# Kernel tuning notes

Measured on AMD Instinct MI355X. Metric: run time of the kernel, lower is better.

Reference implementation:

```python
import jax, jax.numpy as jnp
import numpy as np

NUM_HEADS = 16
HEAD_DIM = 64  # v_emb_out // num_heads


def setup_inputs() -> dict:
    key = jax.random.key(0)
    ks = jax.random.split(key, 12)
    B, QL, KL = 2, 2048, 2048
    D = 1024  # q_emb_in = k_emb_in = v_emb_in = v_emb_out
    s = 0.02
    return {
        "q": jax.random.normal(ks[0], (B, QL, D), jnp.float32),
        "k": jax.random.normal(ks[1], (B, KL, D), jnp.float32),
        "v": jax.random.normal(ks[2], (B, KL, D), jnp.float32),
        "mask": jnp.zeros((B, 1, 1, KL), jnp.int32),
        "Wq": jax.random.normal(ks[3], (D, D), jnp.float32) * s,
        "bq": jnp.zeros((D,), jnp.float32),
        "Wk": jax.random.normal(ks[4], (D, D), jnp.float32) * s,
        "bk": jnp.zeros((D,), jnp.float32),
        "Wv": jax.random.normal(ks[5], (D, D), jnp.float32) * s,
        "bv": jnp.zeros((D,), jnp.float32),
        "Wo": jax.random.normal(ks[6], (D, D), jnp.float32) * s,
        "bo": jnp.zeros((D,), jnp.float32),
    }


def _split_heads(x):
    # (B, S, D) -> (B, H, S, Hd)
    B, S, D = x.shape
    return x.reshape(B, S, NUM_HEADS, HEAD_DIM).transpose(0, 2, 1, 3)


def reference(q, k, v, mask, Wq, bq, Wk, bk, Wv, bv, Wo, bo):
    Q = _split_heads(q @ Wq.T + bq)
    K = _split_heads(k @ Wk.T + bk)
    V = _split_heads(v @ Wv.T + bv)
    scores = jnp.einsum("bhqd,bhkd->bhqk", Q, K) / jnp.sqrt(
        jnp.asarray(HEAD_DIM, Q.dtype)
    )
    scores = jnp.where(mask.astype(bool), jnp.asarray(-jnp.inf, scores.dtype), scores)
    attn = jax.nn.softmax(scores, axis=-1)
    out = jnp.einsum("bhqk,bhkd->bhqd", attn, V)  # (B,H,Q,Hd)
    B, H, QL, Hd = out.shape
    out = out.transpose(0, 2, 1, 3).reshape(B, QL, H * Hd)
    return out @ Wo.T + bo
```

## Files before the change

### kernel.cpp

```cpp
#include <hip/hip_runtime.h>
#include <hip/hip_bf16.h>
#include <math.h>
#include <stdint.h>


typedef __bf16 bf16x8 __attribute__((ext_vector_type(8)));
typedef float  f32x4  __attribute__((ext_vector_type(4)));
typedef float  f32x8  __attribute__((ext_vector_type(8)));
typedef unsigned short u16x8 __attribute__((ext_vector_type(8)));
typedef unsigned short u16x4 __attribute__((ext_vector_type(4)));
typedef u16x8 u16x8a __attribute__((may_alias));
typedef u16x4 u16x4a __attribute__((may_alias));
typedef f32x8 f32x8a __attribute__((may_alias));
typedef unsigned short u16a __attribute__((may_alias));
typedef float f32a __attribute__((may_alias));

#define BATCH 2
#define SQL   2048
#define DM    1024
#define NH    16
#define HD    64

__device__ __forceinline__ unsigned short f2bf(float f) {
    union { __hip_bfloat16 h; unsigned short u; } cv;
    cv.h = __float2bfloat16(f);
    return cv.u;
}
__device__ __forceinline__ float bf2f(unsigned short u) {
    union { unsigned int i; float f; } cv;
    cv.i = ((unsigned int)u) << 16;
    return cv.f;
}
__device__ __forceinline__ bf16x8 ldfrag(const unsigned short* p) {
    return __builtin_bit_cast(bf16x8, *(const u16x8a*)p);
}
__device__ __forceinline__ void stage8(const void* __restrict__ src, size_t off,
                                       int f32f, unsigned short* dst) {
    if (f32f) {
        f32x8 v = *(const f32x8a*)((const float*)src + off);
        u16x8 o;
#pragma unroll
        for (int i = 0; i < 8; i++) o[i] = f2bf(v[i]);
        *(u16x8a*)dst = o;
    } else {
        *(u16x8a*)dst = *(const u16x8a*)((const unsigned short*)src + off);
    }
}
__device__ __forceinline__ float rdel(const void* p, size_t i, int f) {
    return f ? ((const f32a*)p)[i] : bf2f(((const u16a*)p)[i]);
}
__device__ __forceinline__ void gload16(const void* g, void* l) {
    __builtin_amdgcn_global_load_lds(
        (const __attribute__((address_space(1))) unsigned int*)g,
        (__attribute__((address_space(3))) unsigned int*)l,
        16, 0, 0);
}

__global__ void sniff(const void* __restrict__ q, int* __restrict__ flag) {
    __shared__ int cnt;
    if (threadIdx.x == 0) cnt = 0;
    __syncthreads();
    const u16a* p = (const u16a*)q;
    int c = 0;
#pragma unroll
    for (int i = 0; i < 8; i++) {
        unsigned short u = p[threadIdx.x * 8 + i];
        int e = (u >> 7) & 0xFF;
        if (e >= 96 && e <= 159) c++;
    }
    atomicAdd(&cnt, c);
    __syncthreads();
    if (threadIdx.x == 0) *flag = (cnt < 1741) ? 1 : 0;
}

__global__ __launch_bounds__(256)
void convert(const void* s0, const void* s1, const void* s2, const void* s3,
             const void* s4, const void* s5, const void* s6,
             unsigned short* d0, unsigned short* d1, unsigned short* d2,
             unsigned short* d3, unsigned short* d4, unsigned short* d5,
             unsigned short* d6, const int* __restrict__ flag)
{
    if (*flag == 0) return;
    const int z = blockIdx.z;
    const float* s; unsigned short* d; size_t n;
    switch (z) {
        case 0: s = (const float*)s0; d = d0; n = (size_t)BATCH * SQL * DM; break;
        case 1: s = (const float*)s1; d = d1; n = (size_t)BATCH * SQL * DM; break;
        case 2: s = (const float*)s2; d = d2; n = (size_t)BATCH * SQL * DM; break;
        case 3: s = (const float*)s3; d = d3; n = (size_t)DM * DM; break;
        case 4: s = (const float*)s4; d = d4; n = (size_t)DM * DM; break;
        case 5: s = (const float*)s5; d = d5; n = (size_t)DM * DM; break;
        default: s = (const float*)s6; d = d6; n = (size_t)DM * DM; break;
    }
    const size_t stride = (size_t)gridDim.x * blockDim.x * 8;
    for (size_t i = ((size_t)blockIdx.x * blockDim.x + threadIdx.x) * 8; i < n;
         i += stride) {
        f32x8 v = *(const f32x8a*)(s + i);
        u16x8 o;
#pragma unroll
        for (int j = 0; j < 8; j++) o[j] = f2bf(v[j]);
        *(u16x8a*)(d + i) = o;
    }
}

template<int BLDS, int BN>
__device__ __forceinline__ void gemm_core(
    const unsigned short* __restrict__ Abf,
    const unsigned short* __restrict__ Bbf,
    const void* __restrict__ Braw,
    const void* __restrict__ bias, void* __restrict__ Cv,
    float scale, int wF32, int oMode, int bF32)
{
    constexpr int K = 1024, N = 1024, BK = 32;
    constexpr int NJ = BN / 32;
    constexpr int CALLS = BN / 64;
    __shared__ unsigned short Alds[128 * BK];
    __shared__ unsigned short Blds[BN * BK];

    const int t = threadIdx.x;
    const int lane = t & 63, wave = t >> 6;
    const int quad = lane >> 4, r15 = lane & 15;
    const int wm = (wave >> 1) * 64, wn = (wave & 1) * (BN / 2);
    const int m0 = blockIdx.x * 128, n0 = blockIdx.y * BN;

    f32x4 acc[4][NJ];
#pragma unroll
    for (int i = 0; i < 4; i++)
#pragma unroll
        for (int j = 0; j < NJ; j++) acc[i][j] = (f32x4){0.f, 0.f, 0.f, 0.f};

    const int gr = lane >> 2, gc = lane & 3;
    const unsigned short* gA = Abf + (size_t)(m0 + wave * 32 + gr) * K + gc * 8;
    const unsigned short* gB = Bbf + (size_t)(n0 + wave * 16 * CALLS + gr) * K + gc * 8;
    unsigned short* lA = &Alds[wave * 1024];
    unsigned short* lB = &Blds[wave * 512 * CALLS];
    const int srow = t >> 2, sch = t & 3;
    const size_t offB0 = (size_t)(n0 + srow) * K + sch * 8;
    const size_t offB1 = (size_t)(n0 + 64 + srow) * K + sch * 8;

    for (int k0 = 0; k0 < K; k0 += BK) {
        gload16(gA + k0, lA);
        gload16(gA + k0 + 16 * K, lA + 512);
        if constexpr (BLDS) {
#pragma unroll
            for (int c = 0; c < CALLS; c++)
                gload16(gB + k0 + c * 16 * K, lB + c * 512);
        } else {
            stage8(Braw, offB0 + k0, wF32, &Blds[srow * BK + sch * 8]);
            if constexpr (BN == 128)
                stage8(Braw, offB1 + k0, wF32, &Blds[(64 + srow) * BK + sch * 8]);
        }
        __syncthreads();

        bf16x8 af[4], bfr[NJ];
#pragma unroll
        for (int i = 0; i < 4; i++)
            af[i] = ldfrag(&Alds[(wm + i * 16 + r15) * BK + quad * 8]);
#pragma unroll
        for (int j = 0; j < NJ; j++)
            bfr[j] = ldfrag(&Blds[(wn + j * 16 + r15) * BK + quad * 8]);
#pragma unroll
        for (int i = 0; i < 4; i++)
#pragma unroll
            for (int j = 0; j < NJ; j++)
                acc[i][j] = __builtin_amdgcn_mfma_f32_16x16x32_bf16(af[i], bfr[j], acc[i][j], 0, 0, 0);
        __syncthreads();
    }

    float bvv[NJ];
#pragma unroll
    for (int j = 0; j < NJ; j++)
        bvv[j] = rdel(bias, n0 + wn + j * 16 + r15, bF32);

    if (oMode == 2) {
#pragma unroll
        for (int i = 0; i < 4; i++)
#pragma unroll
            for (int j = 0; j < NJ; j++) {
                int rr = m0 + wm + i * 16 + quad * 4;
                int cc = n0 + wn + j * 16 + r15;
                int bb = rr >> 11, tok = rr & (SQL - 1);
                int hh = cc >> 6,  dd  = cc & (HD - 1);
                u16x4 pk;
#pragma unroll
                for (int r = 0; r < 4; r++) pk[r] = f2bf(acc[i][j][r] + bvv[j]);
                *(u16x4a*)&((u16a*)Cv)[((((size_t)bb * NH + hh) * HD + dd) << 11) + tok] = pk;
            }
    } else {
#pragma unroll
        for (int i = 0; i < 4; i++)
#pragma unroll
            for (int j = 0; j < NJ; j++)
#pragma unroll
                for (int r = 0; r < 4; r++) {
                    int rr = m0 + wm + i * 16 + quad * 4 + r;
                    int cc = n0 + wn + j * 16 + r15;
                    float vv = (acc[i][j][r] + bvv[j]) * scale;
                    if (oMode) ((f32a*)Cv)[(size_t)rr * N + cc] = vv;
                    else       ((u16a*)Cv)[(size_t)rr * N + cc] = f2bf(vv);
                }
    }
}

template<int BLDS>
__global__ __launch_bounds__(256)
void gemm_qkv_k(const void* __restrict__ xq, const void* __restrict__ xk,
                const void* __restrict__ xv,
                const unsigned short* __restrict__ qc,
                const unsigned short* __restrict__ kc,
                const unsigned short* __restrict__ vc,
                const void* __restrict__ Wq, const void* __restrict__ Wk,
                const void* __restrict__ Wv,
                const unsigned short* __restrict__ Wqc,
                const unsigned short* __restrict__ Wkc,
                const unsigned short* __restrict__ Wvc,
                const void* __restrict__ bq, const void* __restrict__ bk,
                const void* __restrict__ bv,
                unsigned short* __restrict__ Qp, unsigned short* __restrict__ Kp,
                unsigned short* __restrict__ Vp,
                float qscale, const int* __restrict__ flag)
{
    const int f = *flag;
    const int z = blockIdx.z;
    const void* xo = (z == 0) ? xq : (z == 1) ? xk : xv;
    const unsigned short* xc = (z == 0) ? qc : (z == 1) ? kc : vc;
    const unsigned short* A = f ? xc : (const unsigned short*)xo;
    const void* Wraw = (z == 0) ? Wq : (z == 1) ? Wk : Wv;
    const unsigned short* Wc = (z == 0) ? Wqc : (z == 1) ? Wkc : Wvc;
    const unsigned short* Bc = (BLDS && f) ? Wc : (const unsigned short*)Wraw;
    const void* bi = (z == 0) ? bq : (z == 1) ? bk : bv;
    unsigned short* C = (z == 0) ? Qp : (z == 1) ? Kp : Vp;
    gemm_core<BLDS, 128>(A, Bc, Wraw, bi, C, (z == 0) ? qscale : 1.0f, f,
                         (z == 2) ? 2 : 0, f);
}

template<int BLDS>
__global__ __launch_bounds__(256)
void gemm_o_k(const unsigned short* __restrict__ A, const void* __restrict__ Wo,
              const unsigned short* __restrict__ Woc, const void* __restrict__ bo,
              void* __restrict__ out, const int* __restrict__ flag)
{
    const int f = *flag;
    const unsigned short* Bc = (BLDS && f) ? Woc : (const unsigned short*)Wo;
    gemm_core<BLDS, 64>(A, Bc, Wo, bo, out, 1.0f, f, f, f);
}

__global__ __launch_bounds__(256)
void flash(const unsigned short* __restrict__ Qp,
           const unsigned short* __restrict__ Kp,
           const unsigned short* __restrict__ VT,
           const int* __restrict__ mask,
           unsigned short* __restrict__ AO)
{
    __shared__ unsigned short Klds[2][64 * 64];
    __shared__ unsigned short Vlds[2][64 * 64];
    __shared__ unsigned short Plds[4][32 * 72];

    const int t = threadIdx.x, wave = t >> 6, lane = t & 63;
    const int quad = lane >> 4, r15 = lane & 15;
    const int x7 = r15 & 7;
    const int qt = blockIdx.x, bh = blockIdx.y, b = bh >> 4, h = bh & 15;
    const size_t base = (size_t)b * SQL * DM + (size_t)h * HD;

    const int srow8 = lane >> 3, sc8 = lane & 7;
    const unsigned short* gK[2];
    const unsigned short* gV[2];
    int ldof[2];
#pragma unroll
    for (int i = 0; i < 2; i++) {
        const int row = wave * 16 + i * 8 + srow8;
        const int slot = sc8 ^ (row & 7);
        gK[i] = Kp + base + (size_t)row * DM + slot * 8;
        gV[i] = VT + (((size_t)(b * NH + h) * HD + row) << 11) + slot * 8;
        ldof[i] = (wave * 16 + i * 8) * 64;
    }

    bf16x8 qf[2][2];
#pragma unroll
    for (int g = 0; g < 2; g++) {
        const int qrow = qt * 128 + wave * 32 + g * 16 + r15;
        qf[g][0] = ldfrag(&Qp[base + (size_t)qrow * DM + quad * 8]);
        qf[g][1] = ldfrag(&Qp[base + (size_t)qrow * DM + 32 + quad * 8]);
    }

    f32x4 o[2][4];
#pragma unroll
    for (int g = 0; g < 2; g++)
#pragma unroll
        for (int jd = 0; jd < 4; jd++) o[g][jd] = (f32x4){0.f, 0.f, 0.f, 0.f};
    float l_i[2][4] = {{0.f, 0.f, 0.f, 0.f}, {0.f, 0.f, 0.f, 0.f}};

#pragma unroll
    for (int i = 0; i < 2; i++) {
        gload16(gK[i], &Klds[0][ldof[i]]);
        gload16(gV[i], &Vlds[0][ldof[i]]);
    }
    __syncthreads();

    constexpr int NT = SQL / 64;
    for (int it = 0; it < NT; ++it) {
        const int bs = it & 1;
        const int n0 = it * 64;

        int mraw[4];
#pragma unroll
        for (int j = 0; j < 4; j++)
            mraw[j] = mask[b * SQL + n0 + j * 16 + r15];

        if (it + 1 < NT) {
#pragma unroll
            for (int i = 0; i < 2; i++) {
                gload16(gK[i] + (size_t)(n0 + 64) * DM, &Klds[bs ^ 1][ldof[i]]);
                gload16(gV[i] + (n0 + 64),              &Vlds[bs ^ 1][ldof[i]]);
            }
        }

        f32x4 s4[2][4];
#pragma unroll
        for (int g = 0; g < 2; g++)
#pragma unroll
            for (int j = 0; j < 4; j++) s4[g][j] = (f32x4){0.f, 0.f, 0.f, 0.f};
#pragma unroll
        for (int j = 0; j < 4; j++) {
            const int row = j * 16 + r15;
            bf16x8 kf0 = ldfrag(&Klds[bs][row * 64 + ((quad ^ x7) << 3)]);
            bf16x8 kf1 = ldfrag(&Klds[bs][row * 64 + (((4 + quad) ^ x7) << 3)]);
#pragma unroll
            for (int g = 0; g < 2; g++) {
                s4[g][j] = __builtin_amdgcn_mfma_f32_16x16x32_bf16(qf[g][0], kf0, s4[g][j], 0, 0, 0);
                s4[g][j] = __builtin_amdgcn_mfma_f32_16x16x32_bf16(qf[g][1], kf1, s4[g][j], 0, 0, 0);
            }
        }

#pragma unroll
        for (int j = 0; j < 4; j++) {
            const float mval = (mraw[j] != 0) ? -INFINITY : 0.f;
#pragma unroll
            for (int g = 0; g < 2; g++)
#pragma unroll
                for (int r = 0; r < 4; r++) {
                    float p = exp2f(s4[g][j][r] + mval);
                    l_i[g][r] += p;
                    Plds[wave][(g * 16 + quad * 4 + r) * 72 + j * 16 + r15] = f2bf(p);
                }
        }
        asm volatile("" ::: "memory");

#pragma unroll
        for (int kf = 0; kf < 2; kf++) {
            bf16x8 pa0 = ldfrag(&Plds[wave][(r15) * 72 + kf * 32 + quad * 8]);
            bf16x8 pa1 = ldfrag(&Plds[wave][(16 + r15) * 72 + kf * 32 + quad * 8]);
#pragma unroll
            for (int jd = 0; jd < 4; jd++) {
                const int row = jd * 16 + r15;
                bf16x8 vb8 = ldfrag(
                    &Vlds[bs][row * 64 + (((kf * 4 + quad) ^ x7) << 3)]);
                o[0][jd] = __builtin_amdgcn_mfma_f32_16x16x32_bf16(pa0, vb8, o[0][jd], 0, 0, 0);
                o[1][jd] = __builtin_amdgcn_mfma_f32_16x16x32_bf16(pa1, vb8, o[1][jd], 0, 0, 0);
            }
        }
        __syncthreads();
    }

#pragma unroll
    for (int off = 1; off < 16; off <<= 1)
#pragma unroll
        for (int g = 0; g < 2; g++)
#pragma unroll
            for (int r = 0; r < 4; r++)
                l_i[g][r] += __shfl_xor(l_i[g][r], off, 64);
#pragma unroll
    for (int g = 0; g < 2; g++)
#pragma unroll
        for (int r = 0; r < 4; r++)
            l_i[g][r] = (l_i[g][r] > 0.f) ? 1.0f / l_i[g][r] : 0.f;

#pragma unroll
    for (int g = 0; g < 2; g++)
#pragma unroll
        for (int jd = 0; jd < 4; jd++)
#pragma unroll
            for (int r = 0; r < 4; r++) {
                int row = qt * 128 + wave * 32 + g * 16 + quad * 4 + r;
                AO[base + (size_t)row * DM + jd * 16 + r15] =
                    f2bf(o[g][jd][r] * l_i[g][r]);
            }
}

extern "C" void kernel_launch(void* const* d_in, const int* in_sizes, int n_in,
                              void* d_out, int out_size, void* d_ws, size_t ws_size,
                              hipStream_t stream)
{
    (void)in_sizes; (void)n_in; (void)out_size;

    const void* q    = d_in[0];
    const void* k    = d_in[1];
    const void* v    = d_in[2];
    const int*  mask = (const int*)d_in[3];
    const void* Wq   = d_in[4];
    const void* bq   = d_in[5];
    const void* Wk   = d_in[6];
    const void* bk   = d_in[7];
    const void* Wv   = d_in[8];
    const void* bv   = d_in[9];
    const void* Wo   = d_in[10];
    const void* bo   = d_in[11];

    const size_t ACT = (size_t)BATCH * SQL * DM;
    const size_t WE  = (size_t)DM * DM;
    int* flag = (int*)d_ws;
    unsigned short* Qp = (unsigned short*)((char*)d_ws + 512);
    unsigned short* Kp = Qp + ACT;
    unsigned short* Vp = Kp + ACT;
    unsigned short* AO = Vp + ACT;

    const size_t needFull = 512 + (4 * ACT + 3 * ACT + 4 * WE) * 2;
    const size_t needMid  = 512 + (4 * ACT + 4 * WE) * 2;
    const int tier = (ws_size >= needFull) ? 2 : (ws_size >= needMid) ? 1 : 0;

    unsigned short* qc;
    unsigned short* kc;
    unsigned short* vc;
    unsigned short* Wqc = AO + ACT;
    unsigned short* Wkc = Wqc + WE;
    unsigned short* Wvc = Wkc + WE;
    unsigned short* Woc = Wvc + WE;
    if (tier == 2) {
        qc = Woc + WE;
        kc = qc + ACT;
        vc = kc + ACT;
    } else {
        qc = AO;
        kc = (unsigned short*)d_out;
        vc = kc + ACT;
    }

    const float QSCALE = 0.125f * 1.44269504088896340736f;

    sniff<<<1, 256, 0, stream>>>(q, flag);
    if (tier >= 1) {
        convert<<<dim3(256, 1, 7), 256, 0, stream>>>(
            q, k, v, Wq, Wk, Wv, Wo, qc, kc, vc, Wqc, Wkc, Wvc, Woc, flag);
        gemm_qkv_k<1><<<dim3(32, 8, 3), 256, 0, stream>>>(
            q, k, v, qc, kc, vc, Wq, Wk, Wv, Wqc, Wkc, Wvc,
            bq, bk, bv, Qp, Kp, Vp, QSCALE, flag);
    } else {
        convert<<<dim3(256, 1, 3), 256, 0, stream>>>(
            q, k, v, nullptr, nullptr, nullptr, nullptr,
            qc, kc, vc, nullptr, nullptr, nullptr, nullptr, flag);
        gemm_qkv_k<0><<<dim3(32, 8, 3), 256, 0, stream>>>(
            q, k, v, qc, kc, vc, Wq, Wk, Wv, nullptr, nullptr, nullptr,
            bq, bk, bv, Qp, Kp, Vp, QSCALE, flag);
    }
    flash<<<dim3(SQL / 128, BATCH * NH), 256, 0, stream>>>(Qp, Kp, Vp, mask, AO);
    if (tier >= 1)
        gemm_o_k<1><<<dim3(32, 16), 256, 0, stream>>>(AO, Wo, Woc, bo, d_out, flag);
    else
        gemm_o_k<0><<<dim3(32, 16), 256, 0, stream>>>(AO, Wo, nullptr, bo, d_out, flag);
}
```

Measured before the change: 255.0 us.

## Alias bf16 conversion buffers into workspace regions and always use LDS B-loads

Removes the workspace-size tiers and the register-staged B path, reusing dead regions of Qp/Vp/AO/output as scratch for the converted weights and activations so the direct-to-LDS B load path always runs. To make the aliasing safe, the QKV GEMM is split into a Q/K launch and a separate V launch with its own weight conversion, and Wo is converted after flash attention. This adds extra kernel launches and a smaller tile for the V projection in exchange for avoiding the slow fallback when the workspace is small.

```diff
diff --git a/kernel.cpp b/kernel.cpp
--- a/kernel.cpp
+++ b/kernel.cpp
@@ -20,6 +20,8 @@
 #define DM    1024
 #define NH    16
 #define HD    64
+#define ACTN  ((size_t)BATCH * SQL * DM)
+#define WEN   ((size_t)DM * DM)
 
 __device__ __forceinline__ unsigned short f2bf(float f) {
     union { __hip_bfloat16 h; unsigned short u; } cv;
@@ -33,18 +35,6 @@
 }
 __device__ __forceinline__ bf16x8 ldfrag(const unsigned short* p) {
     return __builtin_bit_cast(bf16x8, *(const u16x8a*)p);
-}
-__device__ __forceinline__ void stage8(const void* __restrict__ src, size_t off,
-                                       int f32f, unsigned short* dst) {
-    if (f32f) {
-        f32x8 v = *(const f32x8a*)((const float*)src + off);
-        u16x8 o;
-#pragma unroll
-        for (int i = 0; i < 8; i++) o[i] = f2bf(v[i]);
-        *(u16x8a*)dst = o;
-    } else {
-        *(u16x8a*)dst = *(const u16x8a*)((const unsigned short*)src + off);
-    }
 }
 __device__ __forceinline__ float rdel(const void* p, size_t i, int f) {
     return f ? ((const f32a*)p)[i] : bf2f(((const u16a*)p)[i]);
@@ -74,42 +64,55 @@
 }
 
 __global__ __launch_bounds__(256)
-void convert(const void* s0, const void* s1, const void* s2, const void* s3,
-             const void* s4, const void* s5, const void* s6,
-             unsigned short* d0, unsigned short* d1, unsigned short* d2,
-             unsigned short* d3, unsigned short* d4, unsigned short* d5,
-             unsigned short* d6, const int* __restrict__ flag)
+void convertA(const void* q, const void* k, const void* v,
+              const void* Wq, const void* Wk,
+              unsigned short* qc, unsigned short* kc, unsigned short* vc,
+              unsigned short* Wqc, unsigned short* Wkc,
+              const int* __restrict__ flag)
 {
     if (*flag == 0) return;
     const int z = blockIdx.z;
     const float* s; unsigned short* d; size_t n;
     switch (z) {
-        case 0: s = (const float*)s0; d = d0; n = (size_t)BATCH * SQL * DM; break;
-        case 1: s = (const float*)s1; d = d1; n = (size_t)BATCH * SQL * DM; break;
-        case 2: s = (const float*)s2; d = d2; n = (size_t)BATCH * SQL * DM; break;
-        case 3: s = (const float*)s3; d = d3; n = (size_t)DM * DM; break;
-        case 4: s = (const float*)s4; d = d4; n = (size_t)DM * DM; break;
-        case 5: s = (const float*)s5; d = d5; n = (size_t)DM * DM; break;
-        default: s = (const float*)s6; d = d6; n = (size_t)DM * DM; break;
+        case 0: s = (const float*)q;  d = qc;  n = ACTN; break;
+        case 1: s = (const float*)k;  d = kc;  n = ACTN; break;
+        case 2: s = (const float*)v;  d = vc;  n = ACTN; break;
+        case 3: s = (const float*)Wq; d = Wqc; n = WEN;  break;
+        default: s = (const float*)Wk; d = Wkc; n = WEN; break;
     }
     const size_t stride = (size_t)gridDim.x * blockDim.x * 8;
     for (size_t i = ((size_t)blockIdx.x * blockDim.x + threadIdx.x) * 8; i < n;
          i += stride) {
-        f32x8 v = *(const f32x8a*)(s + i);
+        f32x8 vv = *(const f32x8a*)(s + i);
         u16x8 o;
 #pragma unroll
-        for (int j = 0; j < 8; j++) o[j] = f2bf(v[j]);
+        for (int j = 0; j < 8; j++) o[j] = f2bf(vv[j]);
         *(u16x8a*)(d + i) = o;
     }
 }
 
-template<int BLDS, int BN>
+__global__ __launch_bounds__(256)
+void convertW(const void* s_, unsigned short* d, const int* __restrict__ flag)
+{
+    if (*flag == 0) return;
+    const float* s = (const float*)s_;
+    const size_t stride = (size_t)gridDim.x * blockDim.x * 8;
+    for (size_t i = ((size_t)blockIdx.x * blockDim.x + threadIdx.x) * 8;
+         i < WEN; i += stride) {
+        f32x8 vv = *(const f32x8a*)(s + i);
+        u16x8 o;
+#pragma unroll
+        for (int j = 0; j < 8; j++) o[j] = f2bf(vv[j]);
+        *(u16x8a*)(d + i) = o;
+    }
+}
+
+template<int BN>
 __device__ __forceinline__ void gemm_core(
     const unsigned short* __restrict__ Abf,
     const unsigned short* __restrict__ Bbf,
-    const void* __restrict__ Braw,
     const void* __restrict__ bias, void* __restrict__ Cv,
-    float scale, int wF32, int oMode, int bF32)
+    float scale, int oMode, int bF32)
 {
     constexpr int K = 1024, N = 1024, BK = 32;
     constexpr int NJ = BN / 32;
@@ -134,22 +137,13 @@
     const unsigned short* gB = Bbf + (size_t)(n0 + wave * 16 * CALLS + gr) * K + gc * 8;
     unsigned short* lA = &Alds[wave * 1024];
     unsigned short* lB = &Blds[wave * 512 * CALLS];
-    const int srow = t >> 2, sch = t & 3;
-    const size_t offB0 = (size_t)(n0 + srow) * K + sch * 8;
-    const size_t offB1 = (size_t)(n0 + 64 + srow) * K + sch * 8;
 
     for (int k0 = 0; k0 < K; k0 += BK) {
         gload16(gA + k0, lA);
         gload16(gA + k0 + 16 * K, lA + 512);
-        if constexpr (BLDS) {
-#pragma unroll
-            for (int c = 0; c < CALLS; c++)
-                gload16(gB + k0 + c * 16 * K, lB + c * 512);
-        } else {
-            stage8(Braw, offB0 + k0, wF32, &Blds[srow * BK + sch * 8]);
-            if constexpr (BN == 128)
-                stage8(Braw, offB1 + k0, wF32, &Blds[(64 + srow) * BK + sch * 8]);
-        }
+#pragma unroll
+        for (int c = 0; c < CALLS; c++)
+            gload16(gB + k0 + c * 16 * K, lB + c * 512);
         __syncthreads();
 
         bf16x8 af[4], bfr[NJ];
@@ -202,47 +196,46 @@
     }
 }
 
-template<int BLDS>
-__global__ __launch_bounds__(256)
-void gemm_qkv_k(const void* __restrict__ xq, const void* __restrict__ xk,
-                const void* __restrict__ xv,
-                const unsigned short* __restrict__ qc,
-                const unsigned short* __restrict__ kc,
-                const unsigned short* __restrict__ vc,
-                const void* __restrict__ Wq, const void* __restrict__ Wk,
-                const void* __restrict__ Wv,
-                const unsigned short* __restrict__ Wqc,
-                const unsigned short* __restrict__ Wkc,
-                const unsigned short* __restrict__ Wvc,
-                const void* __restrict__ bq, const void* __restrict__ bk,
-                const void* __restrict__ bv,
-                unsigned short* __restrict__ Qp, unsigned short* __restrict__ Kp,
-                unsigned short* __restrict__ Vp,
-                float qscale, const int* __restrict__ flag)
+__global__ __launch_bounds__(256)
+void gemm_qk(const void* __restrict__ xq, const void* __restrict__ xk,
+             const unsigned short* __restrict__ qc,
+             const unsigned short* __restrict__ kc,
+             const void* __restrict__ Wq, const void* __restrict__ Wk,
+             const unsigned short* __restrict__ Wqc,
+             const unsigned short* __restrict__ Wkc,
+             const void* __restrict__ bq, const void* __restrict__ bk,
+             unsigned short* __restrict__ Qp, unsigned short* __restrict__ Kp,
+             float qscale, const int* __restrict__ flag)
 {
     const int f = *flag;
     const int z = blockIdx.z;
-    const void* xo = (z == 0) ? xq : (z == 1) ? xk : xv;
-    const unsigned short* xc = (z == 0) ? qc : (z == 1) ? kc : vc;
-    const unsigned short* A = f ? xc : (const unsigned short*)xo;
-    const void* Wraw = (z == 0) ? Wq : (z == 1) ? Wk : Wv;
-    const unsigned short* Wc = (z == 0) ? Wqc : (z == 1) ? Wkc : Wvc;
-    const unsigned short* Bc = (BLDS && f) ? Wc : (const unsigned short*)Wraw;
-    const void* bi = (z == 0) ? bq : (z == 1) ? bk : bv;
-    unsigned short* C = (z == 0) ? Qp : (z == 1) ? Kp : Vp;
-    gemm_core<BLDS, 128>(A, Bc, Wraw, bi, C, (z == 0) ? qscale : 1.0f, f,
-                         (z == 2) ? 2 : 0, f);
-}
-
-template<int BLDS>
-__global__ __launch_bounds__(256)
-void gemm_o_k(const unsigned short* __restrict__ A, const void* __restrict__ Wo,
-              const unsigned short* __restrict__ Woc, const void* __restrict__ bo,
-              void* __restrict__ out, const int* __restrict__ flag)
+    const unsigned short* A =
+        f ? (z ? kc : qc) : (const unsigned short*)(z ? xk : xq);
+    const unsigned short* B =
+        f ? (z ? Wkc : Wqc) : (const unsigned short*)(z ? Wk : Wq);
+    gemm_core<128>(A, B, z ? bk : bq, z ? Kp : Qp, z ? 1.0f : qscale, 0, f);
+}
+
+__global__ __launch_bounds__(256)
+void gemm_v(const void* __restrict__ xv, const unsigned short* __restrict__ vc,
+            const void* __restrict__ Wv, const unsigned short* __restrict__ Wvc,
+            const void* __restrict__ bv, unsigned short* __restrict__ VT,
+            const int* __restrict__ flag)
 {
     const int f = *flag;
-    const unsigned short* Bc = (BLDS && f) ? Woc : (const unsigned short*)Wo;
-    gemm_core<BLDS, 64>(A, Bc, Wo, bo, out, 1.0f, f, f, f);
+    const unsigned short* A = f ? vc : (const unsigned short*)xv;
+    const unsigned short* B = f ? Wvc : (const unsigned short*)Wv;
+    gemm_core<64>(A, B, bv, VT, 1.0f, 2, f);
+}
+
+__global__ __launch_bounds__(256)
+void gemm_o(const unsigned short* __restrict__ AO, const void* __restrict__ Wo,
+            const unsigned short* __restrict__ Woc, const void* __restrict__ bo,
+            void* __restrict__ out, const int* __restrict__ flag)
+{
+    const int f = *flag;
+    const unsigned short* B = f ? Woc : (const unsigned short*)Wo;
+    gemm_core<64>(AO, B, bo, out, 1.0f, f, f);
 }
 
 __global__ __launch_bounds__(256)
@@ -391,7 +384,7 @@
                               void* d_out, int out_size, void* d_ws, size_t ws_size,
                               hipStream_t stream)
 {
-    (void)in_sizes; (void)n_in; (void)out_size;
+    (void)in_sizes; (void)n_in; (void)out_size; (void)ws_size;
 
     const void* q    = d_in[0];
     const void* k    = d_in[1];
@@ -406,55 +399,30 @@
     const void* Wo   = d_in[10];
     const void* bo   = d_in[11];
 
-    const size_t ACT = (size_t)BATCH * SQL * DM;
-    const size_t WE  = (size_t)DM * DM;
     int* flag = (int*)d_ws;
     unsigned short* Qp = (unsigned short*)((char*)d_ws + 512);
-    unsigned short* Kp = Qp + ACT;
-    unsigned short* Vp = Kp + ACT;
-    unsigned short* AO = Vp + ACT;
-
-    const size_t needFull = 512 + (4 * ACT + 3 * ACT + 4 * WE) * 2;
-    const size_t needMid  = 512 + (4 * ACT + 4 * WE) * 2;
-    const int tier = (ws_size >= needFull) ? 2 : (ws_size >= needMid) ? 1 : 0;
-
-    unsigned short* qc;
-    unsigned short* kc;
-    unsigned short* vc;
-    unsigned short* Wqc = AO + ACT;
-    unsigned short* Wkc = Wqc + WE;
-    unsigned short* Wvc = Wkc + WE;
-    unsigned short* Woc = Wvc + WE;
-    if (tier == 2) {
-        qc = Woc + WE;
-        kc = qc + ACT;
-        vc = kc + ACT;
-    } else {
-        qc = AO;
-        kc = (unsigned short*)d_out;
-        vc = kc + ACT;
-    }
+    unsigned short* Kp = Qp + ACTN;
+    unsigned short* Vp = Kp + ACTN;
+    unsigned short* AO = Vp + ACTN;
+
+    unsigned short* qc  = AO;
+    unsigned short* kc  = (unsigned short*)d_out;
+    unsigned short* vc  = kc + ACTN;
+    unsigned short* Wqc = Vp;
+    unsigned short* Wkc = Vp + WEN;
+    unsigned short* Wvc = AO;
+    unsigned short* Woc = Qp;
 
     const float QSCALE = 0.125f * 1.44269504088896340736f;
 
     sniff<<<1, 256, 0, stream>>>(q, flag);
-    if (tier >= 1) {
-        convert<<<dim3(256, 1, 7), 256, 0, stream>>>(
-            q, k, v, Wq, Wk, Wv, Wo, qc, kc, vc, Wqc, Wkc, Wvc, Woc, flag);
-        gemm_qkv_k<1><<<dim3(32, 8, 3), 256, 0, stream>>>(
-            q, k, v, qc, kc, vc, Wq, Wk, Wv, Wqc, Wkc, Wvc,
-            bq, bk, bv, Qp, Kp, Vp, QSCALE, flag);
-    } else {
-        convert<<<dim3(256, 1, 3), 256, 0, stream>>>(
-            q, k, v, nullptr, nullptr, nullptr, nullptr,
-            qc, kc, vc, nullptr, nullptr, nullptr, nullptr, flag);
-        gemm_qkv_k<0><<<dim3(32, 8, 3), 256, 0, stream>>>(
-            q, k, v, qc, kc, vc, Wq, Wk, Wv, nullptr, nullptr, nullptr,
-            bq, bk, bv, Qp, Kp, Vp, QSCALE, flag);
-    }
+    convertA<<<dim3(256, 1, 5), 256, 0, stream>>>(
+        q, k, v, Wq, Wk, qc, kc, vc, Wqc, Wkc, flag);
+    gemm_qk<<<dim3(32, 8, 2), 256, 0, stream>>>(
+        q, k, qc, kc, Wq, Wk, Wqc, Wkc, bq, bk, Qp, Kp, QSCALE, flag);
+    convertW<<<dim3(256), 256, 0, stream>>>(Wv, Wvc, flag);
+    gemm_v<<<dim3(32, 16), 256, 0, stream>>>(v, vc, Wv, Wvc, bv, Vp, flag);
     flash<<<dim3(SQL / 128, BATCH * NH), 256, 0, stream>>>(Qp, Kp, Vp, mask, AO);
-    if (tier >= 1)
-        gemm_o_k<1><<<dim3(32, 16), 256, 0, stream>>>(AO, Wo, Woc, bo, d_out, flag);
-    else
-        gemm_o_k<0><<<dim3(32, 16), 256, 0, stream>>>(AO, Wo, nullptr, bo, d_out, flag);
-}
+    convertW<<<dim3(256), 256, 0, stream>>>(Wo, Woc, flag);
+    gemm_o<<<dim3(32, 16), 256, 0, stream>>>(AO, Wo, Woc, bo, d_out, flag);
+}
```

Measured after the change: 277.7 us. +8.9%, slower.

## Double-buffer GEMM LDS tiles to overlap global loads with MFMA

Applied to the files above, without the earlier changes.

Splits the A and B shared-memory tiles into two buffers and prefetches the next K-slice into the alternate buffer while MFMAs run on the current one. This drops one barrier per iteration and aims to hide global-to-LDS load latency behind compute. It doubles LDS use per block, which may lower occupancy. The synchronous stage8 path still blocks on its loads before writing to LDS, so overlap there is limited.

```diff
diff --git a/kernel.cpp b/kernel.cpp
--- a/kernel.cpp
+++ b/kernel.cpp
@@ -114,8 +114,8 @@
     constexpr int K = 1024, N = 1024, BK = 32;
     constexpr int NJ = BN / 32;
     constexpr int CALLS = BN / 64;
-    __shared__ unsigned short Alds[128 * BK];
-    __shared__ unsigned short Blds[BN * BK];
+    __shared__ unsigned short Alds[2][128 * BK];
+    __shared__ unsigned short Blds[2][BN * BK];
 
     const int t = threadIdx.x;
     const int lane = t & 63, wave = t >> 6;
@@ -132,33 +132,52 @@
     const int gr = lane >> 2, gc = lane & 3;
     const unsigned short* gA = Abf + (size_t)(m0 + wave * 32 + gr) * K + gc * 8;
     const unsigned short* gB = Bbf + (size_t)(n0 + wave * 16 * CALLS + gr) * K + gc * 8;
-    unsigned short* lA = &Alds[wave * 1024];
-    unsigned short* lB = &Blds[wave * 512 * CALLS];
+    const int lAo = wave * 1024;
+    const int lBo = wave * 512 * CALLS;
     const int srow = t >> 2, sch = t & 3;
     const size_t offB0 = (size_t)(n0 + srow) * K + sch * 8;
     const size_t offB1 = (size_t)(n0 + 64 + srow) * K + sch * 8;
 
-    for (int k0 = 0; k0 < K; k0 += BK) {
-        gload16(gA + k0, lA);
-        gload16(gA + k0 + 16 * K, lA + 512);
-        if constexpr (BLDS) {
-#pragma unroll
-            for (int c = 0; c < CALLS; c++)
-                gload16(gB + k0 + c * 16 * K, lB + c * 512);
-        } else {
-            stage8(Braw, offB0 + k0, wF32, &Blds[srow * BK + sch * 8]);
-            if constexpr (BN == 128)
-                stage8(Braw, offB1 + k0, wF32, &Blds[(64 + srow) * BK + sch * 8]);
+    gload16(gA, &Alds[0][lAo]);
+    gload16(gA + 16 * K, &Alds[0][lAo + 512]);
+    if constexpr (BLDS) {
+#pragma unroll
+        for (int c = 0; c < CALLS; c++)
+            gload16(gB + c * 16 * K, &Blds[0][lBo + c * 512]);
+    } else {
+        stage8(Braw, offB0, wF32, &Blds[0][srow * BK + sch * 8]);
+        if constexpr (BN == 128)
+            stage8(Braw, offB1, wF32, &Blds[0][(64 + srow) * BK + sch * 8]);
+    }
+    __syncthreads();
+
+    constexpr int NSTEP = K / BK;
+    for (int s = 0; s < NSTEP; ++s) {
+        const int cur = s & 1;
+        if (s + 1 < NSTEP) {
+            const int k0n = (s + 1) * BK;
+            gload16(gA + k0n, &Alds[cur ^ 1][lAo]);
+            gload16(gA + k0n + 16 * K, &Alds[cur ^ 1][lAo + 512]);
+            if constexpr (BLDS) {
+#pragma unroll
+                for (int c = 0; c < CALLS; c++)
+                    gload16(gB + k0n + c * 16 * K, &Blds[cur ^ 1][lBo + c * 512]);
+            } else {
+                stage8(Braw, offB0 + k0n, wF32,
+                       &Blds[cur ^ 1][srow * BK + sch * 8]);
+                if constexpr (BN == 128)
+                    stage8(Braw, offB1 + k0n, wF32,
+                           &Blds[cur ^ 1][(64 + srow) * BK + sch * 8]);
+            }
         }
-        __syncthreads();
 
         bf16x8 af[4], bfr[NJ];
 #pragma unroll
         for (int i = 0; i < 4; i++)
-            af[i] = ldfrag(&Alds[(wm + i * 16 + r15) * BK + quad * 8]);
+            af[i] = ldfrag(&Alds[cur][(wm + i * 16 + r15) * BK + quad * 8]);
 #pragma unroll
         for (int j = 0; j < NJ; j++)
-            bfr[j] = ldfrag(&Blds[(wn + j * 16 + r15) * BK + quad * 8]);
+            bfr[j] = ldfrag(&Blds[cur][(wn + j * 16 + r15) * BK + quad * 8]);
 #pragma unroll
         for (int i = 0; i < 4; i++)
 #pragma unroll
```

Result: slower. 262.6 us (+3.0%).

## Software-pipeline projection GEMM K-loop with multi-buffered LDS and register-staged B

Applied to the files above, without the earlier changes.

Replaces the single-buffered GEMM main loop with a software pipeline. A tiles use a triple-buffered LDS ring filled by direct global-to-LDS loads two steps ahead. B tiles are prefetched into registers and written into a double-buffered LDS slot one step ahead. Explicit vmcnt waits and barriers let global loads overlap the MFMA work instead of stalling on two syncthreads per step. The cost is more LDS per block, more registers for the staged B data, and hand-placed waitcnt counts that must exactly match the number of outstanding loads.

```diff
diff --git a/kernel.cpp b/kernel.cpp
--- a/kernel.cpp
+++ b/kernel.cpp
@@ -33,18 +33,6 @@
 }
 __device__ __forceinline__ bf16x8 ldfrag(const unsigned short* p) {
     return __builtin_bit_cast(bf16x8, *(const u16x8a*)p);
-}
-__device__ __forceinline__ void stage8(const void* __restrict__ src, size_t off,
-                                       int f32f, unsigned short* dst) {
-    if (f32f) {
-        f32x8 v = *(const f32x8a*)((const float*)src + off);
-        u16x8 o;
-#pragma unroll
-        for (int i = 0; i < 8; i++) o[i] = f2bf(v[i]);
-        *(u16x8a*)dst = o;
-    } else {
-        *(u16x8a*)dst = *(const u16x8a*)((const unsigned short*)src + off);
-    }
 }
 __device__ __forceinline__ float rdel(const void* p, size_t i, int f) {
     return f ? ((const f32a*)p)[i] : bf2f(((const u16a*)p)[i]);
@@ -103,69 +91,139 @@
     }
 }
 
-template<int BLDS, int BN>
-__device__ __forceinline__ void gemm_core(
+template<int WF32> struct BRegSel { using T = f32x8; };
+template<> struct BRegSel<0> { using T = u16x8; };
+
+template<int BN, int WF32>
+__device__ __forceinline__ void kloop(
+    unsigned short* __restrict__ Al,
+    unsigned short* __restrict__ Bl,
     const unsigned short* __restrict__ Abf,
-    const unsigned short* __restrict__ Bbf,
-    const void* __restrict__ Braw,
-    const void* __restrict__ bias, void* __restrict__ Cv,
-    float scale, int wF32, int oMode, int bF32)
-{
-    constexpr int K = 1024, N = 1024, BK = 32;
-    constexpr int NJ = BN / 32;
-    constexpr int CALLS = BN / 64;
-    __shared__ unsigned short Alds[128 * BK];
-    __shared__ unsigned short Blds[BN * BK];
-
-    const int t = threadIdx.x;
-    const int lane = t & 63, wave = t >> 6;
+    const void* __restrict__ Bv,
+    f32x4 (&acc)[4][BN / 32], int m0, int n0)
+{
+    constexpr int K = 1024, BK = 32, NJ = BN / 32, NSTEP = K / BK;
+    constexpr int ABUF = 128 * BK, BBUF = BN * BK;
+    constexpr int SV = (BN == 128) ? (WF32 ? 6 : 4) : (WF32 ? 4 : 3);
+    using BR = typename BRegSel<WF32>::T;
+
+    const int tid = threadIdx.x;
+    const int lane = tid & 63, wave = tid >> 6;
     const int quad = lane >> 4, r15 = lane & 15;
     const int wm = (wave >> 1) * 64, wn = (wave & 1) * (BN / 2);
-    const int m0 = blockIdx.x * 128, n0 = blockIdx.y * BN;
-
-    f32x4 acc[4][NJ];
-#pragma unroll
-    for (int i = 0; i < 4; i++)
-#pragma unroll
-        for (int j = 0; j < NJ; j++) acc[i][j] = (f32x4){0.f, 0.f, 0.f, 0.f};
-
     const int gr = lane >> 2, gc = lane & 3;
     const unsigned short* gA = Abf + (size_t)(m0 + wave * 32 + gr) * K + gc * 8;
-    const unsigned short* gB = Bbf + (size_t)(n0 + wave * 16 * CALLS + gr) * K + gc * 8;
-    unsigned short* lA = &Alds[wave * 1024];
-    unsigned short* lB = &Blds[wave * 512 * CALLS];
-    const int srow = t >> 2, sch = t & 3;
+    const int lAo = wave * 1024;
+    const int srow = tid >> 2, sch = tid & 3;
     const size_t offB0 = (size_t)(n0 + srow) * K + sch * 8;
     const size_t offB1 = (size_t)(n0 + 64 + srow) * K + sch * 8;
 
-    for (int k0 = 0; k0 < K; k0 += BK) {
-        gload16(gA + k0, lA);
-        gload16(gA + k0 + 16 * K, lA + 512);
-        if constexpr (BLDS) {
-#pragma unroll
-            for (int c = 0; c < CALLS; c++)
-                gload16(gB + k0 + c * 16 * K, lB + c * 512);
+    auto bload = [&](BR& r0, BR& r1, int kk) {
+        if constexpr (WF32) {
+            r0 = *(const f32x8a*)((const float*)Bv + offB0 + kk);
+            if constexpr (BN == 128)
+                r1 = *(const f32x8a*)((const float*)Bv + offB1 + kk);
         } else {
-            stage8(Braw, offB0 + k0, wF32, &Blds[srow * BK + sch * 8]);
+            r0 = *(const u16x8a*)((const unsigned short*)Bv + offB0 + kk);
             if constexpr (BN == 128)
-                stage8(Braw, offB1 + k0, wF32, &Blds[(64 + srow) * BK + sch * 8]);
+                r1 = *(const u16x8a*)((const unsigned short*)Bv + offB1 + kk);
         }
-        __syncthreads();
-
-        bf16x8 af[4], bfr[NJ];
-#pragma unroll
-        for (int i = 0; i < 4; i++)
-            af[i] = ldfrag(&Alds[(wm + i * 16 + r15) * BK + quad * 8]);
-#pragma unroll
-        for (int j = 0; j < NJ; j++)
-            bfr[j] = ldfrag(&Blds[(wn + j * 16 + r15) * BK + quad * 8]);
-#pragma unroll
-        for (int i = 0; i < 4; i++)
-#pragma unroll
-            for (int j = 0; j < NJ; j++)
-                acc[i][j] = __builtin_amdgcn_mfma_f32_16x16x32_bf16(af[i], bfr[j], acc[i][j], 0, 0, 0);
-        __syncthreads();
-    }
+        (void)r1;
+    };
+    auto bwrite = [&](const BR& r0, const BR& r1, unsigned short* dst) {
+        if constexpr (WF32) {
+            u16x8 o0;
+#pragma unroll
+            for (int i = 0; i < 8; i++) o0[i] = f2bf(r0[i]);
+            *(u16x8a*)&dst[srow * BK + sch * 8] = o0;
+            if constexpr (BN == 128) {
+                u16x8 o1;
+#pragma unroll
+                for (int i = 0; i < 8; i++) o1[i] = f2bf(r1[i]);
+                *(u16x8a*)&dst[(64 + srow) * BK + sch * 8] = o1;
+            }
+        } else {
+            *(u16x8a*)&dst[srow * BK + sch * 8] = __builtin_bit_cast(u16x8, r0);
+            if constexpr (BN == 128)
+                *(u16x8a*)&dst[(64 + srow) * BK + sch * 8] =
+                    __builtin_bit_cast(u16x8, r1);
+        }
+        (void)r1;
+    };
+    auto vmsteady = []() {
+        if constexpr (SV == 6)      asm volatile("s_waitcnt vmcnt(6)" ::: "memory");
+        else if constexpr (SV == 4) asm volatile("s_waitcnt vmcnt(4)" ::: "memory");
+        else                        asm volatile("s_waitcnt vmcnt(3)" ::: "memory");
+    };
+
+    BR rA0{}, rA1{}, rB0{}, rB1{};
+
+    gload16(gA, Al + lAo);
+    gload16(gA + 16 * K, Al + lAo + 512);
+    bload(rA0, rA1, 0);
+    gload16(gA + BK, Al + ABUF + lAo);
+    gload16(gA + BK + 16 * K, Al + ABUF + lAo + 512);
+    bload(rB0, rB1, BK);
+    __builtin_amdgcn_sched_barrier(0);
+    vmsteady();
+    __builtin_amdgcn_sched_barrier(0);
+    bwrite(rA0, rA1, Bl);
+
+#define GSTEP(T_, L0_, L1_, W0_, W1_)                                         \
+    {                                                                         \
+        asm volatile("s_waitcnt lgkmcnt(0)" ::: "memory");                    \
+        __builtin_amdgcn_s_barrier();                                         \
+        __builtin_amdgcn_sched_barrier(0);                                    \
+        const unsigned short* Ab_ = Al + ((T_) % 3) * ABUF;                   \
+        const unsigned short* Bb_ = Bl + ((T_) & 1) * BBUF;                   \
+        bf16x8 af_[4], bf_[NJ];                                               \
+        _Pragma("unroll")                                                     \
+        for (int i = 0; i < 4; i++)                                           \
+            af_[i] = ldfrag(&Ab_[(wm + i * 16 + r15) * BK + quad * 8]);       \
+        _Pragma("unroll")                                                     \
+        for (int j = 0; j < NJ; j++)                                          \
+            bf_[j] = ldfrag(&Bb_[(wn + j * 16 + r15) * BK + quad * 8]);       \
+        _Pragma("unroll")                                                     \
+        for (int i = 0; i < 4; i++)                                           \
+            _Pragma("unroll")                                                 \
+            for (int j = 0; j < NJ; j++)                                      \
+                acc[i][j] = __builtin_amdgcn_mfma_f32_16x16x32_bf16(          \
+                    af_[i], bf_[j], acc[i][j], 0, 0, 0);                      \
+        __builtin_amdgcn_s_barrier();                                         \
+        __builtin_amdgcn_sched_barrier(0);                                    \
+        if ((T_) + 2 < NSTEP) {                                               \
+            const int k2_ = ((T_) + 2) * BK;                                  \
+            unsigned short* Ad_ = Al + (((T_) + 2) % 3) * ABUF;               \
+            gload16(gA + k2_, Ad_ + lAo);                                     \
+            gload16(gA + k2_ + 16 * K, Ad_ + lAo + 512);                      \
+            bload(L0_, L1_, k2_);                                             \
+            __builtin_amdgcn_sched_barrier(0);                                \
+            vmsteady();                                                       \
+            __builtin_amdgcn_sched_barrier(0);                                \
+        } else if ((T_) + 1 < NSTEP) {                                        \
+            asm volatile("s_waitcnt vmcnt(0)" ::: "memory");                  \
+        }                                                                     \
+        if ((T_) + 1 < NSTEP)                                                 \
+            bwrite(W0_, W1_, Bl + (((T_) + 1) & 1) * BBUF);                   \
+    }
+
+    for (int t = 0; t < NSTEP; t += 2) {
+        GSTEP(t,     rA0, rA1, rB0, rB1);
+        GSTEP(t + 1, rB0, rB1, rA0, rA1);
+    }
+#undef GSTEP
+}
+
+template<int BN>
+__device__ __forceinline__ void epilog(
+    f32x4 (&acc)[4][BN / 32], const void* __restrict__ bias,
+    void* __restrict__ Cv, float scale, int oMode, int bF32, int m0, int n0)
+{
+    constexpr int N = 1024, NJ = BN / 32;
+    const int tid = threadIdx.x;
+    const int lane = tid & 63, wave = tid >> 6;
+    const int quad = lane >> 4, r15 = lane & 15;
+    const int wm = (wave >> 1) * 64, wn = (wave & 1) * (BN / 2);
 
     float bvv[NJ];
 #pragma unroll
@@ -202,24 +260,26 @@
     }
 }
 
-template<int BLDS>
 __global__ __launch_bounds__(256)
-void gemm_qkv_k(const void* __restrict__ xq, const void* __restrict__ xk,
-                const void* __restrict__ xv,
-                const unsigned short* __restrict__ qc,
-                const unsigned short* __restrict__ kc,
-                const unsigned short* __restrict__ vc,
-                const void* __restrict__ Wq, const void* __restrict__ Wk,
-                const void* __restrict__ Wv,
-                const unsigned short* __restrict__ Wqc,
-                const unsigned short* __restrict__ Wkc,
-                const unsigned short* __restrict__ Wvc,
-                const void* __restrict__ bq, const void* __restrict__ bk,
-                const void* __restrict__ bv,
-                unsigned short* __restrict__ Qp, unsigned short* __restrict__ Kp,
-                unsigned short* __restrict__ Vp,
-                float qscale, const int* __restrict__ flag)
-{
+void gemm_qkv(const void* __restrict__ xq, const void* __restrict__ xk,
+              const void* __restrict__ xv,
+              const unsigned short* __restrict__ qc,
+              const unsigned short* __restrict__ kc,
+              const unsigned short* __restrict__ vc,
+              const void* __restrict__ Wq, const void* __restrict__ Wk,
+              const void* __restrict__ Wv,
+              const unsigned short* __restrict__ Wqc,
+              const unsigned short* __restrict__ Wkc,
+              const unsigned short* __restrict__ Wvc,
+              const void* __restrict__ bq, const void* __restrict__ bk,
+              const void* __restrict__ bv,
+              unsigned short* __restrict__ Qp, unsigned short* __restrict__ Kp,
+              unsigned short* __restrict__ Vp,
+              float qscale, const int* __restrict__ flag, int useWc)
+{
+    __shared__ unsigned short Al[3 * 128 * 32];
+    __shared__ unsigned short Bl[2 * 128 * 32];
+
     const int f = *flag;
     const int z = blockIdx.z;
     const void* xo = (z == 0) ? xq : (z == 1) ? xk : xv;
@@ -227,22 +287,45 @@
     const unsigned short* A = f ? xc : (const unsigned short*)xo;
     const void* Wraw = (z == 0) ? Wq : (z == 1) ? Wk : Wv;
     const unsigned short* Wc = (z == 0) ? Wqc : (z == 1) ? Wkc : Wvc;
-    const unsigned short* Bc = (BLDS && f) ? Wc : (const unsigned short*)Wraw;
     const void* bi = (z == 0) ? bq : (z == 1) ? bk : bv;
     unsigned short* C = (z == 0) ? Qp : (z == 1) ? Kp : Vp;
-    gemm_core<BLDS, 128>(A, Bc, Wraw, bi, C, (z == 0) ? qscale : 1.0f, f,
-                         (z == 2) ? 2 : 0, f);
-}
-
-template<int BLDS>
+    const float scale = (z == 0) ? qscale : 1.0f;
+    const int oMode = (z == 2) ? 2 : 0;
+    const int m0 = blockIdx.x * 128, n0 = blockIdx.y * 128;
+
+    f32x4 acc[4][4];
+#pragma unroll
+    for (int i = 0; i < 4; i++)
+#pragma unroll
+        for (int j = 0; j < 4; j++) acc[i][j] = (f32x4){0.f, 0.f, 0.f, 0.f};
+
+    if (f && !useWc)      kloop<128, 1>(Al, Bl, A, Wraw, acc, m0, n0);
+    else if (f)           kloop<128, 0>(Al, Bl, A, Wc,   acc, m0, n0);
+    else                  kloop<128, 0>(Al, Bl, A, Wraw, acc, m0, n0);
+    epilog<128>(acc, bi, C, scale, oMode, f, m0, n0);
+}
+
 __global__ __launch_bounds__(256)
-void gemm_o_k(const unsigned short* __restrict__ A, const void* __restrict__ Wo,
-              const unsigned short* __restrict__ Woc, const void* __restrict__ bo,
-              void* __restrict__ out, const int* __restrict__ flag)
-{
+void gemm_o(const unsigned short* __restrict__ A, const void* __restrict__ Wo,
+            const unsigned short* __restrict__ Woc, const void* __restrict__ bo,
+            void* __restrict__ out, const int* __restrict__ flag, int useWc)
+{
+    __shared__ unsigned short Al[3 * 128 * 32];
+    __shared__ unsigned short Bl[2 * 64 * 32];
+
     const int f = *flag;
-    const unsigned short* Bc = (BLDS && f) ? Woc : (const unsigned short*)Wo;
-    gemm_core<BLDS, 64>(A, Bc, Wo, bo, out, 1.0f, f, f, f);
+    const int m0 = blockIdx.x * 128, n0 = blockIdx.y * 64;
+
+    f32x4 acc[4][2];
+#pragma unroll
+    for (int i = 0; i < 4; i++)
+#pragma unroll
+        for (int j = 0; j < 2; j++) acc[i][j] = (f32x4){0.f, 0.f, 0.f, 0.f};
+
+    if (f && !useWc)      kloop<64, 1>(Al, Bl, A, Wo,  acc, m0, n0);
+    else if (f)           kloop<64, 0>(Al, Bl, A, Woc, acc, m0, n0);
+    else                  kloop<64, 0>(Al, Bl, A, Wo,  acc, m0, n0);
+    epilog<64>(acc, bo, out, 1.0f, f, f, m0, n0);
 }
 
 __global__ __launch_bounds__(256)
@@ -434,27 +517,22 @@
         kc = (unsigned short*)d_out;
         vc = kc + ACT;
     }
+    const int useWc = (tier >= 1) ? 1 : 0;
 
     const float QSCALE = 0.125f * 1.44269504088896340736f;
 
     sniff<<<1, 256, 0, stream>>>(q, flag);
-    if (tier >= 1) {
+    if (useWc) {
         convert<<<dim3(256, 1, 7), 256, 0, stream>>>(
             q, k, v, Wq, Wk, Wv, Wo, qc, kc, vc, Wqc, Wkc, Wvc, Woc, flag);
-        gemm_qkv_k<1><<<dim3(32, 8, 3), 256, 0, stream>>>(
-            q, k, v, qc, kc, vc, Wq, Wk, Wv, Wqc, Wkc, Wvc,
-            bq, bk, bv, Qp, Kp, Vp, QSCALE, flag);
     } else {
         convert<<<dim3(256, 1, 3), 256, 0, stream>>>(
             q, k, v, nullptr, nullptr, nullptr, nullptr,
             qc, kc, vc, nullptr, nullptr, nullptr, nullptr, flag);
-        gemm_qkv_k<0><<<dim3(32, 8, 3), 256, 0, stream>>>(
-            q, k, v, qc, kc, vc, Wq, Wk, Wv, nullptr, nullptr, nullptr,
-            bq, bk, bv, Qp, Kp, Vp, QSCALE, flag);
-    }
+    }
+    gemm_qkv<<<dim3(32, 8, 3), 256, 0, stream>>>(
+        q, k, v, qc, kc, vc, Wq, Wk, Wv, Wqc, Wkc, Wvc,
+        bq, bk, bv, Qp, Kp, Vp, QSCALE, flag, useWc);
     flash<<<dim3(SQL / 128, BATCH * NH), 256, 0, stream>>>(Qp, Kp, Vp, mask, AO);
-    if (tier >= 1)
-        gemm_o_k<1><<<dim3(32, 16), 256, 0, stream>>>(AO, Wo, Woc, bo, d_out, flag);
-    else
-        gemm_o_k<0><<<dim3(32, 16), 256, 0, stream>>>(AO, Wo, nullptr, bo, d_out, flag);
-}
+    gemm_o<<<dim3(32, 16), 256, 0, stream>>>(AO, Wo, Woc, bo, d_out, flag, useWc);
+}
```

Result: no change. 257.9 us (+1.2%).
